# Performance work log

Hardware: AMD Instinct MI355X
Metric: run time of the kernel (lower is better)

## Reference

```python
import jax, jax.numpy as jnp
import numpy as np

HEADS = 8
KEY_DIM = 32
EPS = 1e-5


def layernorm(x, gamma, beta, eps=EPS):
    mu = jnp.mean(x, axis=-1, keepdims=True)
    var = jnp.mean(jnp.square(x - mu), axis=-1, keepdims=True)
    return (x - mu) * jax.lax.rsqrt(var + eps) * gamma + beta


def setup_inputs() -> dict:
    key = jax.random.key(0)
    ks = jax.random.split(key, 6)
    B, H, W, C = 16, 32, 32, 256
    inner = HEADS * KEY_DIM  # 256
    s = 1.0 / np.sqrt(C)
    return {
        "x": jax.random.normal(ks[0], (B, H, W, C), jnp.float32),
        "gamma": jnp.ones((C,), jnp.float32),
        "beta": jnp.zeros((C,), jnp.float32),
        "Wq": jax.random.normal(ks[1], (C, inner), jnp.float32) * s,
        "bq": jnp.zeros((inner,), jnp.float32),
        "Wk": jax.random.normal(ks[2], (C, inner), jnp.float32) * s,
        "bk": jnp.zeros((inner,), jnp.float32),
        "Wv": jax.random.normal(ks[3], (C, inner), jnp.float32) * s,
        "bv": jnp.zeros((inner,), jnp.float32),
        "Wp": jax.random.normal(ks[4], (inner, C), jnp.float32) * s,
        "bp": jnp.zeros((C,), jnp.float32),
    }


def reference(x, gamma, beta, Wq, bq, Wk, bk, Wv, bv, Wp, bp):
    B, H, W, C = x.shape
    N = H * W
    h, d = HEADS, KEY_DIM
    X = layernorm(x, gamma, beta)              # [B,H,W,C]
    Xf = X.reshape(B, N, C)                    # 1x1 conv == per-token linear
    Q = (Xf @ Wq + bq).reshape(B, N, h, d)
    K = (Xf @ Wk + bk).reshape(B, N, h, d)
    V = (Xf @ Wv + bv).reshape(B, N, h, d)
    scale = jnp.asarray(d, x.dtype) ** -0.5
    scores = jnp.einsum('bnhd,bmhd->bhnm', Q, K) * scale
    A = jax.nn.softmax(scores, axis=-1)        # [B,h,N,N]
    Y = jnp.einsum('bhnm,bmhd->bnhd', A, V).reshape(B, N, h * d)
    out = (Y @ Wp + bp).reshape(B, H, W, C)
    return out
```

## Files before the change

### kernel.cpp

```cpp
#include <hip/hip_runtime.h>
#include <hip/hip_bf16.h>

typedef __bf16 bf16_t;
typedef __attribute__((ext_vector_type(8))) __bf16 bf16x8;
typedef __attribute__((ext_vector_type(4))) float f32x4;
typedef __attribute__((ext_vector_type(4))) short s16x4;

#define GLDS16(g, l) __builtin_amdgcn_global_load_lds( \
    (const __attribute__((address_space(1))) unsigned int*)(g), \
    (__attribute__((address_space(3))) unsigned int*)(l), 16, 0, 0)

__device__ __forceinline__ float fexp2(float x) {
#if __has_builtin(__builtin_amdgcn_exp2f)
  return __builtin_amdgcn_exp2f(x);
#else
  return exp2f(x);
#endif
}

#define QSCALE (0.17677669529663688f * 1.4426950408889634f)

__global__ __launch_bounds__(256) void lnwtr_kernel(
    const float* __restrict__ x, const float* __restrict__ gamma,
    const float* __restrict__ beta, bf16_t* __restrict__ Xln,
    const float* __restrict__ Wq, const float* __restrict__ Wk,
    const float* __restrict__ Wv, const float* __restrict__ Wp,
    bf16_t* __restrict__ Wt)
{
  if (blockIdx.x < 1024) {
    const int idx = blockIdx.x * 256 + threadIdx.x;
    const int mat = idx >> 16;
    const int e   = idx & 65535;
    const int k   = e >> 8;
    const int n   = e & 255;
    const float* W = (mat == 0) ? Wq : (mat == 1) ? Wk : (mat == 2) ? Wv : Wp;
    Wt[(size_t)mat * 65536 + n * 256 + k] = (bf16_t)W[e];
    return;
  }
  const int wave = threadIdx.x >> 6, lane = threadIdx.x & 63;
  const int tok = (blockIdx.x - 1024) * 4 + wave;
  const float4 v = *reinterpret_cast<const float4*>(x + (size_t)tok * 256 + lane * 4);
  float s1 = v.x + v.y + v.z + v.w;
  float s2 = v.x*v.x + v.y*v.y + v.z*v.z + v.w*v.w;
  #pragma unroll
  for (int off = 1; off < 64; off <<= 1) {
    s1 += __shfl_xor(s1, off);
    s2 += __shfl_xor(s2, off);
  }
  const float mean = s1 * (1.0f/256.0f);
  const float var  = s2 * (1.0f/256.0f) - mean*mean;
  const float rstd = rsqrtf(var + 1e-5f);
  const float4 g  = *reinterpret_cast<const float4*>(gamma + lane*4);
  const float4 be = *reinterpret_cast<const float4*>(beta  + lane*4);
  union { bf16_t h4[4]; unsigned long long u; } pk;
  pk.h4[0] = (bf16_t)((v.x-mean)*rstd*g.x + be.x);
  pk.h4[1] = (bf16_t)((v.y-mean)*rstd*g.y + be.y);
  pk.h4[2] = (bf16_t)((v.z-mean)*rstd*g.z + be.z);
  pk.h4[3] = (bf16_t)((v.w-mean)*rstd*g.w + be.w);
  *reinterpret_cast<unsigned long long*>(Xln + (size_t)tok*256 + lane*4) = pk.u;
}

__global__ __launch_bounds__(256) void gemm0_kernel(
    const bf16_t* __restrict__ A, const bf16_t* __restrict__ Wt,
    const float* __restrict__ b0, const float* __restrict__ b1,
    const float* __restrict__ b2,
    bf16_t* __restrict__ Qb, bf16_t* __restrict__ Kb, bf16_t* __restrict__ Vt)
{
  __shared__ __align__(16) bf16_t As[128*64];
  __shared__ __align__(16) bf16_t Bs[128*64];
  const int tid  = threadIdx.x;
  const int lane = tid & 63, wave = tid >> 6;
  const int lg = lane >> 4, li = lane & 15;
  const int wm = wave >> 1, wn = wave & 1;
  const int mt = blockIdx.x;
  const int nt = blockIdx.y;
  const int mat = nt >> 1, nbase = (nt & 1) * 128;
  const bf16_t* Bm = Wt + (size_t)mat * 65536;

  f32x4 acc[4][4] = {};

  for (int kt = 0; kt < 4; ++kt) {
    __syncthreads();
    #pragma unroll
    for (int i = 0; i < 4; ++i) {
      const int idx = i*256 + tid;
      const int row = idx >> 3, ck = idx & 7;
      const int cs = ck ^ (row & 7);
      GLDS16(A + (size_t)(mt*128 + row)*256 + kt*64 + cs*8, As + idx*8);
    }
    #pragma unroll
    for (int i = 0; i < 4; ++i) {
      const int idx = i*256 + tid;
      const int row = idx >> 3, ck = idx & 7;
      const int cs = ck ^ (row & 7);
      GLDS16(Bm + (size_t)(nbase + row)*256 + kt*64 + cs*8, Bs + idx*8);
    }
    __syncthreads();
    #pragma unroll
    for (int kk = 0; kk < 2; ++kk) {
      bf16x8 af[4], bfv[4];
      #pragma unroll
      for (int mi = 0; mi < 4; ++mi) {
        const int row = wm*64 + mi*16 + li;
        const int c = (kk*4 + lg) ^ (row & 7);
        af[mi] = *reinterpret_cast<const bf16x8*>(As + row*64 + c*8);
      }
      #pragma unroll
      for (int ni = 0; ni < 4; ++ni) {
        const int row = wn*64 + ni*16 + li;
        const int c = (kk*4 + lg) ^ (row & 7);
        bfv[ni] = *reinterpret_cast<const bf16x8*>(Bs + row*64 + c*8);
      }
      #pragma unroll
      for (int mi = 0; mi < 4; ++mi)
        #pragma unroll
        for (int ni = 0; ni < 4; ++ni)
          acc[mi][ni] = __builtin_amdgcn_mfma_f32_16x16x32_bf16(af[mi], bfv[ni], acc[mi][ni], 0, 0, 0);
    }
  }

  const float* bias = (mat == 0) ? b0 : (mat == 1) ? b1 : b2;
  if (mat < 2) {
    bf16_t* Out = (mat == 0) ? Qb : Kb;
    const float osc = (mat == 0) ? QSCALE : 1.0f;
    #pragma unroll
    for (int mi = 0; mi < 4; ++mi)
      #pragma unroll
      for (int ni = 0; ni < 4; ++ni) {
        const int col = nbase + wn*64 + ni*16 + li;
        const float bb = bias[col];
        #pragma unroll
        for (int r = 0; r < 4; ++r) {
          const int row = mt*128 + wm*64 + mi*16 + lg*4 + r;
          Out[(size_t)row*256 + col] = (bf16_t)((acc[mi][ni][r] + bb) * osc);
        }
      }
  } else {
    #pragma unroll
    for (int mi = 0; mi < 4; ++mi)
      #pragma unroll
      for (int ni = 0; ni < 4; ++ni) {
        const int col = nbase + wn*64 + ni*16 + li;
        const int hh = col >> 5, dd = col & 31;
        const float bb = bias[col];
        const int row0 = mt*128 + wm*64 + mi*16 + lg*4;
        const int bi = row0 >> 10, nn = row0 & 1023;
        union { bf16_t h4[4]; unsigned long long u; } pk;
        #pragma unroll
        for (int r = 0; r < 4; ++r) pk.h4[r] = (bf16_t)(acc[mi][ni][r] + bb);
        *reinterpret_cast<unsigned long long*>(
            Vt + ((size_t)(bi*8 + hh)*32 + dd)*1024 + nn) = pk.u;
      }
  }
}

__global__ __launch_bounds__(256) void gemm1_kernel(
    const bf16_t* __restrict__ A, const bf16_t* __restrict__ Wt,
    const float* __restrict__ b0, float* __restrict__ Fout)
{
  __shared__ __align__(16) bf16_t As[64*64];
  __shared__ __align__(16) bf16_t Bs[64*64];
  const int tid  = threadIdx.x;
  const int lane = tid & 63, wave = tid >> 6;
  const int lg = lane >> 4, li = lane & 15;
  const int wm = wave >> 1, wn = wave & 1;
  const int mt = blockIdx.x;
  const int nbase = blockIdx.y * 64;

  f32x4 acc[2][2] = {};

  for (int kt = 0; kt < 4; ++kt) {
    __syncthreads();
    #pragma unroll
    for (int i = 0; i < 2; ++i) {
      const int idx = i*256 + tid;
      const int row = idx >> 3, ck = idx & 7;
      const int cs = ck ^ (row & 7);
      GLDS16(A + (size_t)(mt*64 + row)*256 + kt*64 + cs*8, As + idx*8);
    }
    #pragma unroll
    for (int i = 0; i < 2; ++i) {
      const int idx = i*256 + tid;
      const int row = idx >> 3, ck = idx & 7;
      const int cs = ck ^ (row & 7);
      GLDS16(Wt + (size_t)(nbase + row)*256 + kt*64 + cs*8, Bs + idx*8);
    }
    __syncthreads();
    #pragma unroll
    for (int kk = 0; kk < 2; ++kk) {
      bf16x8 af[2], bfv[2];
      #pragma unroll
      for (int mi = 0; mi < 2; ++mi) {
        const int row = wm*32 + mi*16 + li;
        const int c = (kk*4 + lg) ^ (row & 7);
        af[mi] = *reinterpret_cast<const bf16x8*>(As + row*64 + c*8);
      }
      #pragma unroll
      for (int ni = 0; ni < 2; ++ni) {
        const int row = wn*32 + ni*16 + li;
        const int c = (kk*4 + lg) ^ (row & 7);
        bfv[ni] = *reinterpret_cast<const bf16x8*>(Bs + row*64 + c*8);
      }
      #pragma unroll
      for (int mi = 0; mi < 2; ++mi)
        #pragma unroll
        for (int ni = 0; ni < 2; ++ni)
          acc[mi][ni] = __builtin_amdgcn_mfma_f32_16x16x32_bf16(af[mi], bfv[ni], acc[mi][ni], 0, 0, 0);
    }
  }

  #pragma unroll
  for (int mi = 0; mi < 2; ++mi)
    #pragma unroll
    for (int ni = 0; ni < 2; ++ni) {
      const int col = nbase + wn*32 + ni*16 + li;
      const float bb = b0[col];
      #pragma unroll
      for (int r = 0; r < 4; ++r) {
        const int row = mt*64 + wm*32 + mi*16 + lg*4 + r;
        Fout[(size_t)row*256 + col] = acc[mi][ni][r] + bb;
      }
    }
}

__global__ __launch_bounds__(512, 8) void attn_kernel(
    const bf16_t* __restrict__ Qb, const bf16_t* __restrict__ Kb,
    const bf16_t* __restrict__ Vt, bf16_t* __restrict__ Yb)
{
  __shared__ __align__(16) char Ks[3][4096];
  __shared__ __align__(16) char Vs[3][4096];
  const int tid  = threadIdx.x;
  const int wave = tid >> 6, lane = tid & 63;
  const int lg = lane >> 4, li = lane & 15;
  const int gid = blockIdx.x;
  const int qt = (gid >> 3) & 7;
  const int bh = ((gid >> 6) << 3) | (gid & 7);
  const int b  = bh >> 3, hh = bh & 7;
  const int tok0 = b*1024 + qt*128 + wave*16;

  const bf16x8 qf = *reinterpret_cast<const bf16x8*>(
      Qb + (size_t)(tok0 + li)*256 + hh*32 + lg*8);

  const bf16_t* Ssrc;
  if (tid < 256) {
    const int s = tid, ktok = s >> 2, ks = s & 3;
    Ssrc = Kb + (size_t)(b*1024 + ktok)*256 + hh*32 + ((ks ^ ((ktok >> 1) & 3)) * 8);
  } else {
    const int s = tid - 256, vd = s >> 3, vs = s & 7;
    Ssrc = Vt + ((size_t)bh*32 + vd)*1024 + ((vs ^ (vd & 7)) * 8);
  }
  const size_t sstride = (tid < 256) ? (size_t)16384 : (size_t)64;
  const int sloff = (tid < 256) ? tid*16 : (tid-256)*16;
  char* sbase = (tid < 256) ? &Ks[0][0] : &Vs[0][0];

  const int kof = li*64 + ((lg ^ ((li >> 1) & 3)) * 16);
  int vof[4];
  #pragma unroll
  for (int ct = 0; ct < 4; ++ct)
    vof[ct] = li*128 + (((ct*2 + (lg >> 1)) ^ (li & 7)) * 16) + (lg & 1)*8;

  const f32x4 fz = {0.f, 0.f, 0.f, 0.f};
  f32x4 acc0 = fz, acc1 = fz;
  f32x4 accl = fz;

  const short oneb = 0x3F80;
  const s16x4 vone = {oneb, oneb, oneb, oneb};

  GLDS16(Ssrc,           sbase + sloff);
  GLDS16(Ssrc + sstride, sbase + 4096 + sloff);

  #pragma unroll
  for (int mc = 0; mc < 16; ++mc) {
    if (mc < 15) asm volatile("s_waitcnt vmcnt(1)" ::: "memory");
    else         asm volatile("s_waitcnt vmcnt(0)" ::: "memory");
    __builtin_amdgcn_s_barrier();
    asm volatile("" ::: "memory");
    if (mc + 2 < 16)
      GLDS16(Ssrc + (size_t)(mc+2)*sstride, sbase + ((mc+2)%3)*4096 + sloff);
    const char* kb = &Ks[mc%3][0];
    const char* vb = &Vs[mc%3][0];
    f32x4 s[4];
    __builtin_amdgcn_s_setprio(1);
    #pragma unroll
    for (int ct = 0; ct < 4; ++ct) {
      const bf16x8 kfrag = *reinterpret_cast<const bf16x8*>(kb + kof + ct*1024);
      s[ct] = __builtin_amdgcn_mfma_f32_16x16x32_bf16(kfrag, qf, fz, 0, 0, 0);
    }
    __builtin_amdgcn_s_setprio(0);
    #pragma unroll
    for (int ct = 0; ct < 4; ++ct) {
      union { bf16_t h4[4]; s16x4 v; } pk;
      #pragma unroll
      for (int r = 0; r < 4; ++r) pk.h4[r] = (bf16_t)fexp2(s[ct][r]);
      const s16x4 vq0 = *reinterpret_cast<const s16x4*>(vb + vof[ct]);
      const s16x4 vq1 = *reinterpret_cast<const s16x4*>(vb + vof[ct] + 16*128);
      __builtin_amdgcn_s_setprio(1);
      acc0 = __builtin_amdgcn_mfma_f32_16x16x16bf16_1k(vq0,  pk.v, acc0, 0, 0, 0);
      acc1 = __builtin_amdgcn_mfma_f32_16x16x16bf16_1k(vq1,  pk.v, acc1, 0, 0, 0);
      accl = __builtin_amdgcn_mfma_f32_16x16x16bf16_1k(vone, pk.v, accl, 0, 0, 0);
      __builtin_amdgcn_s_setprio(0);
    }
  }

  const float inv = 1.0f / accl[0];
  union { bf16_t h4[4]; unsigned long long u; } o0, o1;
  #pragma unroll
  for (int r = 0; r < 4; ++r) {
    o0.h4[r] = (bf16_t)(acc0[r]*inv);
    o1.h4[r] = (bf16_t)(acc1[r]*inv);
  }
  bf16_t* yp = Yb + (size_t)(tok0 + li)*256 + hh*32;
  *reinterpret_cast<unsigned long long*>(yp + lg*4)      = o0.u;
  *reinterpret_cast<unsigned long long*>(yp + 16 + lg*4) = o1.u;
}

extern "C" void kernel_launch(void* const* d_in, const int* in_sizes, int n_in,
                              void* d_out, int out_size, void* d_ws, size_t ws_size,
                              hipStream_t stream) {
  const float* x     = (const float*)d_in[0];
  const float* gamma = (const float*)d_in[1];
  const float* beta  = (const float*)d_in[2];
  const float* Wq    = (const float*)d_in[3];
  const float* bq    = (const float*)d_in[4];
  const float* Wk    = (const float*)d_in[5];
  const float* bk    = (const float*)d_in[6];
  const float* Wv    = (const float*)d_in[7];
  const float* bv    = (const float*)d_in[8];
  const float* Wp    = (const float*)d_in[9];
  const float* bp    = (const float*)d_in[10];
  float* out = (float*)d_out;

  char* ws = (char*)d_ws;
  bf16_t* Wt  = (bf16_t*)(ws);
  bf16_t* Xln = (bf16_t*)(ws + 524288);
  bf16_t* Qb  = (bf16_t*)(ws + 8912896);
  bf16_t* Kb  = (bf16_t*)(ws + 17301504);
  bf16_t* Vt  = (bf16_t*)(ws + 25690112);
  bf16_t* Yb  = Xln;

  lnwtr_kernel<<<5120, 256, 0, stream>>>(x, gamma, beta, Xln,
                                         Wq, Wk, Wv, Wp, Wt);
  gemm0_kernel<<<dim3(128, 6), 256, 0, stream>>>(
      Xln, Wt, bq, bk, bv, Qb, Kb, Vt);
  attn_kernel<<<1024, 512, 0, stream>>>(Qb, Kb, Vt, Yb);
  gemm1_kernel<<<dim3(256, 4), 256, 0, stream>>>(
      Yb, Wt + 3*65536, bp, out);
}
```

Measured before the change: 64.96 us.

## Triple-buffer QKV GEMM LDS tiles with async global-to-LDS prefetch

Reworks the QKV projection GEMM main loop from four single-buffered K=64 stages into eight K=32 stages over a three-slot LDS ring. Prefetch runs two stages ahead, guarded by explicit vmcnt waits and one barrier per stage, so global loads overlap MFMA work. It also changes the XOR swizzle for 32-wide rows and raises wave priority around the MFMA block. The cost is more barriers and smaller per-stage MFMA bursts, with correctness depending on the hand-placed waitcnt values.

```diff
diff --git a/kernel.cpp b/kernel.cpp
--- a/kernel.cpp
+++ b/kernel.cpp
@@ -66,8 +66,8 @@
     const float* __restrict__ b2,
     bf16_t* __restrict__ Qb, bf16_t* __restrict__ Kb, bf16_t* __restrict__ Vt)
 {
-  __shared__ __align__(16) bf16_t As[128*64];
-  __shared__ __align__(16) bf16_t Bs[128*64];
+  __shared__ __align__(16) bf16_t As[3][128*32];
+  __shared__ __align__(16) bf16_t Bs[3][128*32];
   const int tid  = threadIdx.x;
   const int lane = tid & 63, wave = tid >> 6;
   const int lg = lane >> 4, li = lane & 15;
@@ -77,46 +77,64 @@
   const int mat = nt >> 1, nbase = (nt & 1) * 128;
   const bf16_t* Bm = Wt + (size_t)mat * 65536;
 
+  const bf16_t* Asrc[2];
+  const bf16_t* Bsrc[2];
+  int dsto[2];
+  #pragma unroll
+  for (int i = 0; i < 2; ++i) {
+    const int idx = i*256 + tid;
+    const int row = idx >> 2, slot = idx & 3;
+    const int cs = slot ^ ((row >> 1) & 3);
+    Asrc[i] = A  + (size_t)(mt*128 + row)*256 + cs*8;
+    Bsrc[i] = Bm + (size_t)(nbase + row)*256 + cs*8;
+    dsto[i] = idx * 8;
+  }
+
   f32x4 acc[4][4] = {};
 
-  for (int kt = 0; kt < 4; ++kt) {
-    __syncthreads();
-    #pragma unroll
-    for (int i = 0; i < 4; ++i) {
-      const int idx = i*256 + tid;
-      const int row = idx >> 3, ck = idx & 7;
-      const int cs = ck ^ (row & 7);
-      GLDS16(A + (size_t)(mt*128 + row)*256 + kt*64 + cs*8, As + idx*8);
-    }
-    #pragma unroll
-    for (int i = 0; i < 4; ++i) {
-      const int idx = i*256 + tid;
-      const int row = idx >> 3, ck = idx & 7;
-      const int cs = ck ^ (row & 7);
-      GLDS16(Bm + (size_t)(nbase + row)*256 + kt*64 + cs*8, Bs + idx*8);
-    }
-    __syncthreads();
-    #pragma unroll
-    for (int kk = 0; kk < 2; ++kk) {
-      bf16x8 af[4], bfv[4];
-      #pragma unroll
-      for (int mi = 0; mi < 4; ++mi) {
-        const int row = wm*64 + mi*16 + li;
-        const int c = (kk*4 + lg) ^ (row & 7);
-        af[mi] = *reinterpret_cast<const bf16x8*>(As + row*64 + c*8);
-      }
-      #pragma unroll
-      for (int ni = 0; ni < 4; ++ni) {
-        const int row = wn*64 + ni*16 + li;
-        const int c = (kk*4 + lg) ^ (row & 7);
-        bfv[ni] = *reinterpret_cast<const bf16x8*>(Bs + row*64 + c*8);
-      }
-      #pragma unroll
-      for (int mi = 0; mi < 4; ++mi)
-        #pragma unroll
-        for (int ni = 0; ni < 4; ++ni)
-          acc[mi][ni] = __builtin_amdgcn_mfma_f32_16x16x32_bf16(af[mi], bfv[ni], acc[mi][ni], 0, 0, 0);
-    }
+  #pragma unroll
+  for (int s = 0; s < 2; ++s) {
+    GLDS16(Asrc[0] + s*32, &As[s][dsto[0]]);
+    GLDS16(Bsrc[0] + s*32, &Bs[s][dsto[0]]);
+    GLDS16(Asrc[1] + s*32, &As[s][dsto[1]]);
+    GLDS16(Bsrc[1] + s*32, &Bs[s][dsto[1]]);
+  }
+
+  #pragma unroll
+  for (int kt = 0; kt < 8; ++kt) {
+    if (kt < 7) asm volatile("s_waitcnt vmcnt(4)" ::: "memory");
+    else        asm volatile("s_waitcnt vmcnt(0)" ::: "memory");
+    __builtin_amdgcn_s_barrier();
+    asm volatile("" ::: "memory");
+    if (kt + 2 < 8) {
+      const int rb = (kt + 2) % 3;
+      GLDS16(Asrc[0] + (kt+2)*32, &As[rb][dsto[0]]);
+      GLDS16(Bsrc[0] + (kt+2)*32, &Bs[rb][dsto[0]]);
+      GLDS16(Asrc[1] + (kt+2)*32, &As[rb][dsto[1]]);
+      GLDS16(Bsrc[1] + (kt+2)*32, &Bs[rb][dsto[1]]);
+    }
+    const bf16_t* as_ = As[kt % 3];
+    const bf16_t* bs_ = Bs[kt % 3];
+    bf16x8 af[4], bfv[4];
+    #pragma unroll
+    for (int mi = 0; mi < 4; ++mi) {
+      const int row = wm*64 + mi*16 + li;
+      const int c = lg ^ ((row >> 1) & 3);
+      af[mi] = *reinterpret_cast<const bf16x8*>(as_ + row*32 + c*8);
+    }
+    #pragma unroll
+    for (int ni = 0; ni < 4; ++ni) {
+      const int row = wn*64 + ni*16 + li;
+      const int c = lg ^ ((row >> 1) & 3);
+      bfv[ni] = *reinterpret_cast<const bf16x8*>(bs_ + row*32 + c*8);
+    }
+    __builtin_amdgcn_s_setprio(1);
+    #pragma unroll
+    for (int mi = 0; mi < 4; ++mi)
+      #pragma unroll
+      for (int ni = 0; ni < 4; ++ni)
+        acc[mi][ni] = __builtin_amdgcn_mfma_f32_16x16x32_bf16(af[mi], bfv[ni], acc[mi][ni], 0, 0, 0);
+    __builtin_amdgcn_s_setprio(0);
   }
 
   const float* bias = (mat == 0) ? b0 : (mat == 1) ? b1 : b2;
```

Result: no change. 65.76 us (+1.2%).
